# Optimization experiments

Hardware: AMD Instinct MI355X
Metric: run time of the kernel (lower is better)

The kernel has to match this reference:

```python
import jax, jax.numpy as jnp
import numpy as np

USER_NUM = 100000
ITEM_NUM = 100000
EMB = 128
N_USERS = 65536
N_BEH = 2097152
N_GROUPS = 2048


def setup_inputs() -> dict:
    key = jax.random.key(0)
    ks = jax.random.split(key, 7)
    user_ids = jax.random.randint(ks[0], (N_USERS,), 0, USER_NUM, dtype=jnp.int32)
    user_group_ids = jnp.sort(jax.random.randint(ks[1], (N_USERS,), 0, N_GROUPS, dtype=jnp.int32))
    behavior_item_ids = jax.random.randint(ks[2], (N_BEH,), 0, ITEM_NUM, dtype=jnp.int32)
    behavior_counts = jax.random.uniform(ks[3], (N_BEH,), dtype=jnp.float32)
    behavior_user_ids = jnp.sort(jax.random.randint(ks[4], (N_BEH,), 0, N_USERS, dtype=jnp.int32))
    user_table = jax.random.normal(ks[5], (USER_NUM, EMB), dtype=jnp.float32)
    item_table = jax.random.normal(ks[6], (ITEM_NUM, EMB), dtype=jnp.float32)
    return {
        "user_ids": user_ids,
        "user_group_ids": user_group_ids,
        "behavior_item_ids": behavior_item_ids,
        "behavior_counts": behavior_counts,
        "behavior_user_ids": behavior_user_ids,
        "user_table": user_table,
        "item_table": item_table,
        "num_groups": N_GROUPS,
    }


def reference(user_ids, user_group_ids, behavior_item_ids, behavior_counts,
              behavior_user_ids, user_table, item_table, num_groups):
    n_users = user_ids.shape[0]
    # weighted bag-of-items per user: sum_j item_emb[b_id] * count  -> [n_users, EMB]
    beh_emb = item_table[behavior_item_ids] * behavior_counts[:, None]
    per_user_beh = jax.ops.segment_sum(beh_emb, behavior_user_ids, num_segments=n_users)
    # user embedding with padding_idx=0 (id 0 -> zero vector)
    ue = user_table[user_ids] * (user_ids != 0).astype(user_table.dtype)[:, None]
    per_user = per_user_beh * ue  # personalized behavior embedding
    # pooling == 'sum' over users within each group -> [num_groups, EMB]
    group_embedding = jax.ops.segment_sum(per_user, user_group_ids, num_segments=num_groups)
    return group_embedding
```

## Files before the change

### kernel.cpp

```cpp
#include <hip/hip_runtime.h>
#include <hip/hip_fp16.h>

#define EMB 128

__global__ __launch_bounds__(256) void prep_kernel(
    const float* __restrict__ src, __half* __restrict__ dst, int n8,
    const int* __restrict__ beh_user, int* __restrict__ start,
    int n_beh, int n_users)
{
    int t = blockIdx.x * 256 + threadIdx.x;
    if (t < n8) {
        const float4* s = (const float4*)src + (size_t)t * 2;
        float4 f0 = s[0];
        float4 f1 = s[1];
        union { __half h[8]; uint4 u; } pk;
        pk.h[0] = __float2half_rn(f0.x); pk.h[1] = __float2half_rn(f0.y);
        pk.h[2] = __float2half_rn(f0.z); pk.h[3] = __float2half_rn(f0.w);
        pk.h[4] = __float2half_rn(f1.x); pk.h[5] = __float2half_rn(f1.y);
        pk.h[6] = __float2half_rn(f1.z); pk.h[7] = __float2half_rn(f1.w);
        ((uint4*)dst)[t] = pk.u;
    }
    if (t < n_beh) {
        int cur  = beh_user[t];
        int prev = (t == 0) ? -1 : beh_user[t - 1];
        if (cur != prev) {
            for (int u = prev + 1; u <= cur; ++u) start[u] = t;
        }
        if (t == n_beh - 1) {
            for (int u = cur + 1; u <= n_users; ++u) start[u] = n_beh;
        }
    }
}

#define ACCUM(W_, c)                                              \
    {                                                             \
        float2 f01 = __half22float2(*(const __half2*)&(W_).x);    \
        float2 f23 = __half22float2(*(const __half2*)&(W_).y);    \
        float2 f45 = __half22float2(*(const __half2*)&(W_).z);    \
        float2 f67 = __half22float2(*(const __half2*)&(W_).w);    \
        a0 = fmaf(f01.x, (c), a0); a1 = fmaf(f01.y, (c), a1);     \
        a2 = fmaf(f23.x, (c), a2); a3 = fmaf(f23.y, (c), a3);     \
        a4 = fmaf(f45.x, (c), a4); a5 = fmaf(f45.y, (c), a5);     \
        a6 = fmaf(f67.x, (c), a6); a7 = fmaf(f67.y, (c), a7);     \
    }

__global__ __launch_bounds__(256) void per_user_kernel(
    const int*    __restrict__ user_ids,
    const int*    __restrict__ group_ids,
    const int*    __restrict__ beh_item,
    const float*  __restrict__ beh_cnt,
    const float*  __restrict__ user_table,
    const __half* __restrict__ item_f16,
    const int*    __restrict__ start,
    float*        __restrict__ out,
    int n_users)
{
    const int lane = threadIdx.x & 63;
    const int q    = lane >> 4;
    const int r    = lane & 15;
    const int wave = threadIdx.x >> 6;
    const int user = blockIdx.x * 4 + wave;

    __shared__ float lds_acc[EMB];
    __shared__ int   lds_grp[4];
    if (threadIdx.x < EMB) lds_acc[threadIdx.x] = 0.0f;

    float a0 = 0.f, a1 = 0.f, a2 = 0.f, a3 = 0.f;
    float a4 = 0.f, a5 = 0.f, a6 = 0.f, a7 = 0.f;
    int g = -1;

    if (user < n_users) {
        const int s = start[user];
        const int e = start[user + 1];

        const __half* itp = item_f16 + r * 8;

        int   idx_c = 0;
        float cnt_c = 0.f;
        {
            int t0 = s + r;
            if (t0 < e) { idx_c = beh_item[t0]; cnt_c = beh_cnt[t0]; }
        }

        for (int j = s; j < e; j += 16) {
            int   idx_n = 0;
            float cnt_n = 0.f;
            int   tn = j + 16 + r;
            if (tn < e) { idx_n = beh_item[tn]; cnt_n = beh_cnt[tn]; }

            int   bi0 = __shfl(idx_c, q * 4 + 0, 16);
            int   bi1 = __shfl(idx_c, q * 4 + 1, 16);
            int   bi2 = __shfl(idx_c, q * 4 + 2, 16);
            int   bi3 = __shfl(idx_c, q * 4 + 3, 16);
            float c0  = __shfl(cnt_c, q * 4 + 0, 16);
            float c1  = __shfl(cnt_c, q * 4 + 1, 16);
            float c2  = __shfl(cnt_c, q * 4 + 2, 16);
            float c3  = __shfl(cnt_c, q * 4 + 3, 16);

            uint4 w0 = *(const uint4*)(itp + (size_t)bi0 * EMB);
            uint4 w1 = *(const uint4*)(itp + (size_t)bi1 * EMB);
            uint4 w2 = *(const uint4*)(itp + (size_t)bi2 * EMB);
            uint4 w3 = *(const uint4*)(itp + (size_t)bi3 * EMB);

            ACCUM(w0, c0);
            ACCUM(w1, c1);
            ACCUM(w2, c2);
            ACCUM(w3, c3);

            idx_c = idx_n;
            cnt_c = cnt_n;
        }

        a0 += __shfl_xor(a0, 16, 64); a1 += __shfl_xor(a1, 16, 64);
        a2 += __shfl_xor(a2, 16, 64); a3 += __shfl_xor(a3, 16, 64);
        a4 += __shfl_xor(a4, 16, 64); a5 += __shfl_xor(a5, 16, 64);
        a6 += __shfl_xor(a6, 16, 64); a7 += __shfl_xor(a7, 16, 64);
        a0 += __shfl_xor(a0, 32, 64); a1 += __shfl_xor(a1, 32, 64);
        a2 += __shfl_xor(a2, 32, 64); a3 += __shfl_xor(a3, 32, 64);
        a4 += __shfl_xor(a4, 32, 64); a5 += __shfl_xor(a5, 32, 64);
        a6 += __shfl_xor(a6, 32, 64); a7 += __shfl_xor(a7, 32, 64);

        const int uid = user_ids[user];
        if (uid != 0) {
            const float* up = user_table + (size_t)uid * EMB + r * 8;
            float4 u0 = *(const float4*)up;
            float4 u1 = *(const float4*)(up + 4);
            a0 *= u0.x; a1 *= u0.y; a2 *= u0.z; a3 *= u0.w;
            a4 *= u1.x; a5 *= u1.y; a6 *= u1.z; a7 *= u1.w;
        } else {
            a0 = a1 = a2 = a3 = a4 = a5 = a6 = a7 = 0.f;
        }

        g = group_ids[user];
    }

    float v0, v1;
    if      (q == 0) { v0 = a0; v1 = a1; }
    else if (q == 1) { v0 = a2; v1 = a3; }
    else if (q == 2) { v0 = a4; v1 = a5; }
    else             { v0 = a6; v1 = a7; }
    const int d0 = r * 8 + q * 2;

    if (lane == 0) lds_grp[wave] = g;
    __syncthreads();

    const int g0 = lds_grp[0];
    const bool same = (g0 >= 0) && (lds_grp[1] == g0) &&
                      (lds_grp[2] == g0) && (lds_grp[3] == g0);
    if (same) {
        atomicAdd(&lds_acc[d0],     v0);
        atomicAdd(&lds_acc[d0 + 1], v1);
        __syncthreads();
        if (threadIdx.x < 64) {
            const int d = threadIdx.x * 2;
            atomicAdd(&out[(size_t)g0 * EMB + d],     lds_acc[d]);
            atomicAdd(&out[(size_t)g0 * EMB + d + 1], lds_acc[d + 1]);
        }
    } else if (g >= 0) {
        atomicAdd(&out[(size_t)g * EMB + d0],     v0);
        atomicAdd(&out[(size_t)g * EMB + d0 + 1], v1);
    }
}

__global__ __launch_bounds__(256) void per_user_f32_kernel(
    const int*   __restrict__ user_ids,
    const int*   __restrict__ group_ids,
    const int*   __restrict__ beh_item,
    const float* __restrict__ beh_cnt,
    const int*   __restrict__ beh_user,
    const float* __restrict__ user_table,
    const float* __restrict__ item_f32,
    float*       __restrict__ out,
    int n_users, int n_beh)
{
    const int lane = threadIdx.x & 63;
    const int wave = threadIdx.x >> 6;
    const int user = blockIdx.x * 4 + wave;
    float2 acc = make_float2(0.f, 0.f);
    int g = -1;
    if (user < n_users) {
        int lo = 0, hi = n_beh;
        while (lo < hi) { int m = (lo + hi) >> 1; if (beh_user[m] < user) lo = m + 1; else hi = m; }
        int s = lo; hi = n_beh;
        while (lo < hi) { int m = (lo + hi) >> 1; if (beh_user[m] <= user) lo = m + 1; else hi = m; }
        int e = lo;
        for (int j = s; j < e; ++j) {
            int   b = beh_item[j];
            float c = beh_cnt[j];
            float2 v = *(const float2*)(item_f32 + (size_t)b * EMB + lane * 2);
            acc.x = fmaf(v.x, c, acc.x);
            acc.y = fmaf(v.y, c, acc.y);
        }
        int uid = user_ids[user];
        float2 ue = make_float2(0.f, 0.f);
        if (uid != 0) ue = *(const float2*)(user_table + (size_t)uid * EMB + lane * 2);
        acc.x *= ue.x; acc.y *= ue.y;
        g = group_ids[user];
    }
    if (g >= 0) {
        atomicAdd(&out[(size_t)g * EMB + lane * 2],     acc.x);
        atomicAdd(&out[(size_t)g * EMB + lane * 2 + 1], acc.y);
    }
}

extern "C" void kernel_launch(void* const* d_in, const int* in_sizes, int n_in,
                              void* d_out, int out_size, void* d_ws, size_t ws_size,
                              hipStream_t stream) {
    const int*   user_ids   = (const int*)  d_in[0];
    const int*   group_ids  = (const int*)  d_in[1];
    const int*   beh_item   = (const int*)  d_in[2];
    const float* beh_cnt    = (const float*)d_in[3];
    const int*   beh_user   = (const int*)  d_in[4];
    const float* user_table = (const float*)d_in[5];
    const float* item_table = (const float*)d_in[6];

    const int n_users = in_sizes[0];
    const int n_beh   = in_sizes[2];
    const int item_n  = in_sizes[6] / EMB;

    float* out = (float*)d_out;
    (void)hipMemsetAsync(out, 0, (size_t)out_size * sizeof(float), stream);

    size_t start_bytes = (size_t)(n_users + 1) * sizeof(int);
    size_t f16_off     = (start_bytes + 255) & ~(size_t)255;
    size_t f16_bytes   = (size_t)item_n * EMB * sizeof(__half);

    if (ws_size < f16_off + f16_bytes) {
        int ublocks = (n_users + 3) / 4;
        per_user_f32_kernel<<<ublocks, 256, 0, stream>>>(
            user_ids, group_ids, beh_item, beh_cnt, beh_user,
            user_table, item_table, out, n_users, n_beh);
        return;
    }

    int*    start    = (int*)d_ws;
    __half* item_f16 = (__half*)((char*)d_ws + f16_off);

    int n8 = (item_n * EMB) / 8;
    int prep_n = n8 > n_beh ? n8 : n_beh;
    prep_kernel<<<(prep_n + 255) / 256, 256, 0, stream>>>(
        item_table, item_f16, n8, beh_user, start, n_beh, n_users);

    int ublocks = (n_users + 3) / 4;
    per_user_kernel<<<ublocks, 256, 0, stream>>>(
        user_ids, group_ids, beh_item, beh_cnt,
        user_table, item_f16, start, out, n_users);
}
```

Baseline: 233.0 us.

## Software-pipeline item gathers two stages deep and hoist user-row loads

Restructures the per-user gather loop into a three-deep software pipeline: index/count loads run two chunks ahead and the fp16 item-row gathers one chunk ahead of accumulation, so several gathers are in flight per wave. The user embedding row, user id and group id are loaded before the loop so their latency overlaps with the gather work. Behavior index and count loads use nontemporal hints. This raises register pressure and adds rotation copies, which could lower occupancy.

Measured after the change: 228.3 us. 1.02x faster.

```diff
diff --git a/kernel.cpp b/kernel.cpp
--- a/kernel.cpp
+++ b/kernel.cpp
@@ -44,6 +44,16 @@
         a6 = fmaf(f67.x, (c), a6); a7 = fmaf(f67.y, (c), a7);     \
     }
 
+#define SHFL4(DI_, DC_, SI_, SC_)                                 \
+    DI_##0 = __shfl(SI_, q * 4 + 0, 16);                          \
+    DI_##1 = __shfl(SI_, q * 4 + 1, 16);                          \
+    DI_##2 = __shfl(SI_, q * 4 + 2, 16);                          \
+    DI_##3 = __shfl(SI_, q * 4 + 3, 16);                          \
+    DC_##0 = __shfl(SC_, q * 4 + 0, 16);                          \
+    DC_##1 = __shfl(SC_, q * 4 + 1, 16);                          \
+    DC_##2 = __shfl(SC_, q * 4 + 2, 16);                          \
+    DC_##3 = __shfl(SC_, q * 4 + 3, 16);
+
 __global__ __launch_bounds__(256) void per_user_kernel(
     const int*    __restrict__ user_ids,
     const int*    __restrict__ group_ids,
@@ -72,43 +82,74 @@
     if (user < n_users) {
         const int s = start[user];
         const int e = start[user + 1];
-
-        const __half* itp = item_f16 + r * 8;
-
-        int   idx_c = 0;
-        float cnt_c = 0.f;
-        {
-            int t0 = s + r;
-            if (t0 < e) { idx_c = beh_item[t0]; cnt_c = beh_cnt[t0]; }
-        }
-
-        for (int j = s; j < e; j += 16) {
-            int   idx_n = 0;
-            float cnt_n = 0.f;
-            int   tn = j + 16 + r;
-            if (tn < e) { idx_n = beh_item[tn]; cnt_n = beh_cnt[tn]; }
-
-            int   bi0 = __shfl(idx_c, q * 4 + 0, 16);
-            int   bi1 = __shfl(idx_c, q * 4 + 1, 16);
-            int   bi2 = __shfl(idx_c, q * 4 + 2, 16);
-            int   bi3 = __shfl(idx_c, q * 4 + 3, 16);
-            float c0  = __shfl(cnt_c, q * 4 + 0, 16);
-            float c1  = __shfl(cnt_c, q * 4 + 1, 16);
-            float c2  = __shfl(cnt_c, q * 4 + 2, 16);
-            float c3  = __shfl(cnt_c, q * 4 + 3, 16);
-
-            uint4 w0 = *(const uint4*)(itp + (size_t)bi0 * EMB);
-            uint4 w1 = *(const uint4*)(itp + (size_t)bi1 * EMB);
-            uint4 w2 = *(const uint4*)(itp + (size_t)bi2 * EMB);
-            uint4 w3 = *(const uint4*)(itp + (size_t)bi3 * EMB);
-
-            ACCUM(w0, c0);
-            ACCUM(w1, c1);
-            ACCUM(w2, c2);
-            ACCUM(w3, c3);
-
-            idx_c = idx_n;
-            cnt_c = cnt_n;
+        g = group_ids[user];
+
+        const int uid = user_ids[user];
+        float4 u0 = make_float4(0.f, 0.f, 0.f, 0.f);
+        float4 u1 = u0;
+        if (uid != 0) {
+            const float* up = user_table + (size_t)uid * EMB + r * 8;
+            u0 = *(const float4*)up;
+            u1 = *(const float4*)(up + 4);
+        }
+
+        if (s < e) {
+            const __half* itp = item_f16 + r * 8;
+
+            int idxA = 0; float cntA = 0.f;
+            { int t0 = s + r;
+              if (t0 < e) { idxA = __builtin_nontemporal_load(beh_item + t0);
+                            cntA = __builtin_nontemporal_load(beh_cnt + t0); } }
+            int idxB = 0; float cntB = 0.f;
+            { int t1 = s + 16 + r;
+              if (t1 < e) { idxB = __builtin_nontemporal_load(beh_item + t1);
+                            cntB = __builtin_nontemporal_load(beh_cnt + t1); } }
+            int idxC = 0; float cntC = 0.f;
+            { int t2 = s + 32 + r;
+              if (t2 < e) { idxC = __builtin_nontemporal_load(beh_item + t2);
+                            cntC = __builtin_nontemporal_load(beh_cnt + t2); } }
+
+            int aI0, aI1, aI2, aI3; float aC0, aC1, aC2, aC3;
+            SHFL4(aI, aC, idxA, cntA);
+            uint4 wa0 = *(const uint4*)(itp + (size_t)aI0 * EMB);
+            uint4 wa1 = *(const uint4*)(itp + (size_t)aI1 * EMB);
+            uint4 wa2 = *(const uint4*)(itp + (size_t)aI2 * EMB);
+            uint4 wa3 = *(const uint4*)(itp + (size_t)aI3 * EMB);
+
+            int bI0, bI1, bI2, bI3; float bC0, bC1, bC2, bC3;
+            SHFL4(bI, bC, idxB, cntB);
+            uint4 wb0 = *(const uint4*)(itp + (size_t)bI0 * EMB);
+            uint4 wb1 = *(const uint4*)(itp + (size_t)bI1 * EMB);
+            uint4 wb2 = *(const uint4*)(itp + (size_t)bI2 * EMB);
+            uint4 wb3 = *(const uint4*)(itp + (size_t)bI3 * EMB);
+
+            for (int j = s; ; ) {
+                int idxD = 0; float cntD = 0.f;
+                { int t3 = j + 48 + r;
+                  if (t3 < e) { idxD = __builtin_nontemporal_load(beh_item + t3);
+                                cntD = __builtin_nontemporal_load(beh_cnt + t3); } }
+
+                int cI0, cI1, cI2, cI3; float cC0, cC1, cC2, cC3;
+                SHFL4(cI, cC, idxC, cntC);
+                uint4 wc0 = *(const uint4*)(itp + (size_t)cI0 * EMB);
+                uint4 wc1 = *(const uint4*)(itp + (size_t)cI1 * EMB);
+                uint4 wc2 = *(const uint4*)(itp + (size_t)cI2 * EMB);
+                uint4 wc3 = *(const uint4*)(itp + (size_t)cI3 * EMB);
+
+                ACCUM(wa0, aC0);
+                ACCUM(wa1, aC1);
+                ACCUM(wa2, aC2);
+                ACCUM(wa3, aC3);
+
+                j += 16;
+                if (j >= e) break;
+
+                wa0 = wb0; wa1 = wb1; wa2 = wb2; wa3 = wb3;
+                aC0 = bC0; aC1 = bC1; aC2 = bC2; aC3 = bC3;
+                wb0 = wc0; wb1 = wc1; wb2 = wc2; wb3 = wc3;
+                bC0 = cC0; bC1 = cC1; bC2 = cC2; bC3 = cC3;
+                idxC = idxD; cntC = cntD;
+            }
         }
 
         a0 += __shfl_xor(a0, 16, 64); a1 += __shfl_xor(a1, 16, 64);
@@ -120,18 +161,8 @@
         a4 += __shfl_xor(a4, 32, 64); a5 += __shfl_xor(a5, 32, 64);
         a6 += __shfl_xor(a6, 32, 64); a7 += __shfl_xor(a7, 32, 64);
 
-        const int uid = user_ids[user];
-        if (uid != 0) {
-            const float* up = user_table + (size_t)uid * EMB + r * 8;
-            float4 u0 = *(const float4*)up;
-            float4 u1 = *(const float4*)(up + 4);
-            a0 *= u0.x; a1 *= u0.y; a2 *= u0.z; a3 *= u0.w;
-            a4 *= u1.x; a5 *= u1.y; a6 *= u1.z; a7 *= u1.w;
-        } else {
-            a0 = a1 = a2 = a3 = a4 = a5 = a6 = a7 = 0.f;
-        }
-
-        g = group_ids[user];
+        a0 *= u0.x; a1 *= u0.y; a2 *= u0.z; a3 *= u0.w;
+        a4 *= u1.x; a5 *= u1.y; a6 *= u1.z; a7 *= u1.w;
     }
 
     float v0, v1;
```
